# Optimization experiments

Hardware: AMD Instinct MI355X
Metric: run time of the kernel (lower is better)

The kernel has to match this reference:

```python
import jax, jax.numpy as jnp
import numpy as np
from jax import lax

N_HEADS = 10
F_IN = 78
F_OUT = 78           # per-head GAT output dim
HID = N_HEADS * F_OUT  # 780
NEG_SLOPE = 0.2
NUM_GRAPHS = 1024
N_NODES = 40960
N_EDGES = 163840
VOCAB = 26           # CHARPROTLEN + 1
EMB = 128
NFILT = 32
LOUT = 121           # 128 - 8 + 1


def setup_inputs() -> dict:
    key = jax.random.key(0)
    ks = jax.random.split(key, 24)
    d = {}
    d['x'] = jax.random.normal(ks[0], (N_NODES, F_IN), jnp.float32)
    d['edge_index'] = jax.random.randint(ks[1], (2, N_EDGES), 0, N_NODES, jnp.int64)
    d['batch'] = jnp.sort(jax.random.randint(ks[2], (N_NODES,), 0, NUM_GRAPHS, jnp.int64))
    d['target'] = jax.random.randint(ks[3], (NUM_GRAPHS, 1000), 0, VOCAB, jnp.int64)
    s = 0.05
    d['gat_W'] = jax.random.normal(ks[4], (F_IN, HID), jnp.float32) * s
    d['gat_att_src'] = jax.random.normal(ks[5], (N_HEADS, F_OUT), jnp.float32) * s
    d['gat_att_dst'] = jax.random.normal(ks[6], (N_HEADS, F_OUT), jnp.float32) * s
    d['gat_bias'] = jnp.zeros((HID,), jnp.float32)
    d['gcn_W'] = jax.random.normal(ks[7], (HID, HID), jnp.float32) * s
    d['gcn_bias'] = jnp.zeros((HID,), jnp.float32)
    d['fc_g1_W'] = jax.random.normal(ks[8], (2 * HID, 1500), jnp.float32) * s
    d['fc_g1_b'] = jnp.zeros((1500,), jnp.float32)
    d['fc_g2_W'] = jax.random.normal(ks[9], (1500, 128), jnp.float32) * s
    d['fc_g2_b'] = jnp.zeros((128,), jnp.float32)
    d['embed'] = jax.random.normal(ks[10], (VOCAB, EMB), jnp.float32) * s
    d['conv_xt_W'] = jax.random.normal(ks[11], (NFILT, 1000, 8), jnp.float32) * s
    d['conv_xt_b'] = jnp.zeros((NFILT,), jnp.float32)
    d['fc1_xt_W'] = jax.random.normal(ks[12], (NFILT * LOUT, 128), jnp.float32) * s
    d['fc1_xt_b'] = jnp.zeros((128,), jnp.float32)
    d['fc1_W'] = jax.random.normal(ks[13], (256, 1024), jnp.float32) * s
    d['fc1_b'] = jnp.zeros((1024,), jnp.float32)
    d['fc2_W'] = jax.random.normal(ks[14], (1024, 512), jnp.float32) * s
    d['fc2_b'] = jnp.zeros((512,), jnp.float32)
    d['out_W'] = jax.random.normal(ks[15], (512, 1), jnp.float32) * s
    d['out_b'] = jnp.zeros((1,), jnp.float32)
    return d


def _segment_softmax(logits, seg, num_segments):
    m = jax.ops.segment_max(logits, seg, num_segments=num_segments)
    m = jnp.where(jnp.isfinite(m), m, 0.0)
    e = jnp.exp(logits - m[seg])
    s = jax.ops.segment_sum(e, seg, num_segments=num_segments)
    return e / (s[seg] + 1e-16)


def reference(x, edge_index, batch, target, gat_W, gat_att_src, gat_att_dst,
              gat_bias, gcn_W, gcn_bias, fc_g1_W, fc_g1_b, fc_g2_W, fc_g2_b,
              embed, conv_xt_W, conv_xt_b, fc1_xt_W, fc1_xt_b, fc1_W, fc1_b,
              fc2_W, fc2_b, out_W, out_b):
    N = x.shape[0]
    # add self loops (PyG default for both GATConv and GCNConv)
    loops = jnp.arange(N, dtype=edge_index.dtype)
    src = jnp.concatenate([edge_index[0], loops])
    dst = jnp.concatenate([edge_index[1], loops])
    # --- GATConv(78 -> 78, heads=10, concat) ---
    h = (x @ gat_W).reshape(N, N_HEADS, F_OUT)              # [N,10,78]
    a_src = jnp.einsum('nhf,hf->nh', h, gat_att_src)        # [N,10]
    a_dst = jnp.einsum('nhf,hf->nh', h, gat_att_dst)
    logits = jax.nn.leaky_relu(a_src[src] + a_dst[dst], NEG_SLOPE)  # [E',10]
    alpha = _segment_softmax(logits, dst, N)                # softmax over in-edges per dst/head
    agg = jax.ops.segment_sum(h[src] * alpha[:, :, None], dst, num_segments=N)
    x1 = jax.nn.relu(agg.reshape(N, HID) + gat_bias)        # [N,780]
    # --- GCNConv(780 -> 780) with sym normalization ---
    h2 = x1 @ gcn_W
    deg = jax.ops.segment_sum(jnp.ones_like(dst, dtype=h2.dtype), dst, num_segments=N)
    dinv = jnp.where(deg > 0, deg ** -0.5, 0.0)
    norm = dinv[src] * dinv[dst]                            # [E']
    agg2 = jax.ops.segment_sum(h2[src] * norm[:, None], dst, num_segments=N)
    x2 = jax.nn.relu(agg2 + gcn_bias)                       # [N,780]
    # --- global max + mean pool per graph ---
    gmax = jax.ops.segment_max(x2, batch, num_segments=NUM_GRAPHS)
    cnt = jax.ops.segment_sum(jnp.ones((N,), x2.dtype), batch, num_segments=NUM_GRAPHS)
    gmean = jax.ops.segment_sum(x2, batch, num_segments=NUM_GRAPHS) / jnp.maximum(cnt, 1.0)[:, None]
    g = jnp.concatenate([gmax, gmean], axis=1)              # [B,1560]
    g = jax.nn.relu(g @ fc_g1_W + fc_g1_b)
    g = g @ fc_g2_W + fc_g2_b                               # [B,128] (dropout = identity, eval)
    # --- protein branch ---
    e = embed[target]                                       # [B,1000,128]
    conv = lax.conv_general_dilated(e, conv_xt_W, (1,), 'VALID',
                                    dimension_numbers=('NCH', 'OIH', 'NCH'))
    conv = conv + conv_xt_b[None, :, None]                  # [B,32,121]
    xt = conv.reshape(conv.shape[0], NFILT * LOUT) @ fc1_xt_W + fc1_xt_b
    # --- joint head ---
    xc = jnp.concatenate([g, xt], axis=1)                   # [B,256]
    xc = jax.nn.relu(xc @ fc1_W + fc1_b)
    xc = jax.nn.relu(xc @ fc2_W + fc2_b)
    return xc @ out_W + out_b                               # [B,1]
```

## Files before the change

kernel.cpp:

```cpp
#include <hip/hip_runtime.h>

typedef __attribute__((ext_vector_type(4))) float f32x4;
typedef __attribute__((ext_vector_type(8))) short bf16x8;
typedef __attribute__((ext_vector_type(8))) unsigned short u16x8;
typedef unsigned short u16;

#define HID 780
#define NH 10
#define FO 78

__device__ inline u16 f2b(float f) {
  unsigned u = __float_as_uint(f);
  unsigned r = (u + 0x7fff + ((u >> 16) & 1)) >> 16;
  return (u16)r;
}
__device__ inline float b2f(u16 b) { return __uint_as_float(((unsigned)b) << 16); }

__device__ inline void gld16(const u16* g, u16* l) {
  __builtin_amdgcn_global_load_lds(
      (const __attribute__((address_space(1))) unsigned int*)g,
      (__attribute__((address_space(3))) unsigned int*)l, 16, 0, 0);
}

__device__ inline int swz_bid() {
  int gx = gridDim.x, gy = gridDim.y, gz = gridDim.z;
  int nwg = gx * gy * gz;
  int bid = (blockIdx.z * gy + blockIdx.y) * gx + blockIdx.x;
  if ((nwg & 7) == 0) bid = (bid & 7) * (nwg >> 3) + (bid >> 3);
  return bid;
}

template<bool BIAS, bool RELU>
__global__ __launch_bounds__(256) void gemm_mfma(const u16* __restrict__ A,
    const u16* __restrict__ BT, u16* __restrict__ C, float* __restrict__ att_out,
    const float* __restrict__ bias, int M, int Ncols, int KP, int ldc)
{
  __shared__ u16 As[2][128 * 32];
  __shared__ u16 Bs[2][128 * 32];
  const int tid = threadIdx.x;
  int t = swz_bid();
  const int bx = t % gridDim.x, by = t / gridDim.x;
  const int row0 = by << 7, col0 = bx << 7;
  const int l = tid & 63, wid = tid >> 6;
  const int wr = wid >> 1, wc = wid & 1;
  const int lr = l & 15, lk = l >> 4;
  const int c0 = (wid << 6) + l, c1 = 256 + c0;
  const u16* gA0 = A + (size_t)(row0 + (c0 >> 2)) * KP + ((c0 & 3) << 3);
  const u16* gA1 = A + (size_t)(row0 + (c1 >> 2)) * KP + ((c1 & 3) << 3);
  const u16* gB0 = BT + (size_t)(col0 + (c0 >> 2)) * KP + ((c0 & 3) << 3);
  const u16* gB1 = BT + (size_t)(col0 + (c1 >> 2)) * KP + ((c1 & 3) << 3);
  const int d0 = (wid << 6) << 3, d1 = (256 + (wid << 6)) << 3;

  f32x4 acc[4][4];
#pragma unroll
  for (int i = 0; i < 4; ++i)
#pragma unroll
    for (int j = 0; j < 4; ++j) acc[i][j] = (f32x4){0.f, 0.f, 0.f, 0.f};

  gld16(gA0, &As[0][d0]); gld16(gA1, &As[0][d1]);
  gld16(gB0, &Bs[0][d0]); gld16(gB1, &Bs[0][d1]);
  __syncthreads();

  int cur = 0;
  for (int k0 = 0; k0 < KP; k0 += 32) {
    if (k0 + 32 < KP) {
      int nx = cur ^ 1, kn = k0 + 32;
      gld16(gA0 + kn, &As[nx][d0]); gld16(gA1 + kn, &As[nx][d1]);
      gld16(gB0 + kn, &Bs[nx][d0]); gld16(gB1 + kn, &Bs[nx][d1]);
    }
    const u16* Ac = As[cur];
    const u16* Bc = Bs[cur];
    bf16x8 af[4], bfr[4];
#pragma unroll
    for (int fm = 0; fm < 4; ++fm)
      af[fm] = *(const bf16x8*)&Ac[((wr * 64 + fm * 16 + lr) << 5) + (lk << 3)];
#pragma unroll
    for (int fn = 0; fn < 4; ++fn)
      bfr[fn] = *(const bf16x8*)&Bc[((wc * 64 + fn * 16 + lr) << 5) + (lk << 3)];
#pragma unroll
    for (int fm = 0; fm < 4; ++fm)
#pragma unroll
      for (int fn = 0; fn < 4; ++fn)
        acc[fm][fn] = __builtin_amdgcn_mfma_f32_16x16x32_bf16(af[fm], bfr[fn], acc[fm][fn], 0, 0, 0);
    __syncthreads();
    cur ^= 1;
  }
#pragma unroll
  for (int fm = 0; fm < 4; ++fm)
#pragma unroll
    for (int fn = 0; fn < 4; ++fn) {
      int col = col0 + wc * 64 + fn * 16 + lr;
      f32x4 v = acc[fm][fn];
      int rbase = row0 + wr * 64 + fm * 16 + lk * 4;
      if (col < Ncols) {
        float bb = BIAS ? bias[col] : 0.f;
#pragma unroll
        for (int j = 0; j < 4; ++j) {
          float vv = v[j] + bb;
          if (RELU) vv = vv > 0.f ? vv : 0.f;
          C[(size_t)(rbase + j) * ldc + col] = f2b(vv);
        }
      } else {
        if (att_out != nullptr && col < Ncols + 20) {
          int c = col - Ncols;
#pragma unroll
          for (int j = 0; j < 4; ++j)
            att_out[(size_t)(rbase + j) * 20 + c] = v[j];
        }
        if (col < ldc) {
#pragma unroll
          for (int j = 0; j < 4; ++j) C[(size_t)(rbase + j) * ldc + col] = 0;
        }
      }
    }
}

__global__ __launch_bounds__(256) void gemm_sk(const u16* __restrict__ A,
    const u16* __restrict__ BT, float* __restrict__ C,
    int M, int Ncols, int KP, int kchunk)
{
  __shared__ u16 As[2][128 * 32];
  __shared__ u16 Bs[2][128 * 32];
  const int tid = threadIdx.x;
  int t = swz_bid();
  const int bx = t % gridDim.x;
  const int by = (t / gridDim.x) % gridDim.y;
  const int bz = t / (gridDim.x * gridDim.y);
  const int row0 = by << 7, col0 = bx << 7;
  const int kbeg = bz * kchunk;
  const int kend = min(KP, kbeg + kchunk);
  const int l = tid & 63, wid = tid >> 6;
  const int wr = wid >> 1, wc = wid & 1;
  const int lr = l & 15, lk = l >> 4;
  const int c0 = (wid << 6) + l, c1 = 256 + c0;
  const u16* gA0 = A + (size_t)(row0 + (c0 >> 2)) * KP + ((c0 & 3) << 3) + kbeg;
  const u16* gA1 = A + (size_t)(row0 + (c1 >> 2)) * KP + ((c1 & 3) << 3) + kbeg;
  const u16* gB0 = BT + (size_t)(col0 + (c0 >> 2)) * KP + ((c0 & 3) << 3) + kbeg;
  const u16* gB1 = BT + (size_t)(col0 + (c1 >> 2)) * KP + ((c1 & 3) << 3) + kbeg;
  const int d0 = (wid << 6) << 3, d1 = (256 + (wid << 6)) << 3;

  f32x4 acc[4][4];
#pragma unroll
  for (int i = 0; i < 4; ++i)
#pragma unroll
    for (int j = 0; j < 4; ++j) acc[i][j] = (f32x4){0.f, 0.f, 0.f, 0.f};

  gld16(gA0, &As[0][d0]); gld16(gA1, &As[0][d1]);
  gld16(gB0, &Bs[0][d0]); gld16(gB1, &Bs[0][d1]);
  __syncthreads();

  int cur = 0;
  for (int k0 = kbeg; k0 < kend; k0 += 32) {
    if (k0 + 32 < kend) {
      int nx = cur ^ 1, kn = k0 + 32 - kbeg;
      gld16(gA0 + kn, &As[nx][d0]); gld16(gA1 + kn, &As[nx][d1]);
      gld16(gB0 + kn, &Bs[nx][d0]); gld16(gB1 + kn, &Bs[nx][d1]);
    }
    const u16* Ac = As[cur];
    const u16* Bc = Bs[cur];
    bf16x8 af[4], bfr[4];
#pragma unroll
    for (int fm = 0; fm < 4; ++fm)
      af[fm] = *(const bf16x8*)&Ac[((wr * 64 + fm * 16 + lr) << 5) + (lk << 3)];
#pragma unroll
    for (int fn = 0; fn < 4; ++fn)
      bfr[fn] = *(const bf16x8*)&Bc[((wc * 64 + fn * 16 + lr) << 5) + (lk << 3)];
#pragma unroll
    for (int fm = 0; fm < 4; ++fm)
#pragma unroll
      for (int fn = 0; fn < 4; ++fn)
        acc[fm][fn] = __builtin_amdgcn_mfma_f32_16x16x32_bf16(af[fm], bfr[fn], acc[fm][fn], 0, 0, 0);
    __syncthreads();
    cur ^= 1;
  }
#pragma unroll
  for (int fm = 0; fm < 4; ++fm)
#pragma unroll
    for (int fn = 0; fn < 4; ++fn) {
      int col = col0 + wc * 64 + fn * 16 + lr;
      if (col < Ncols) {
        f32x4 v = acc[fm][fn];
        int rbase = row0 + wr * 64 + fm * 16 + lk * 4;
#pragma unroll
        for (int j = 0; j < 4; ++j)
          atomicAdd(&C[(size_t)(rbase + j) * Ncols + col], v[j]);
      }
    }
}

template<bool RELU>
__global__ void bias_act_pad(const float* __restrict__ Cf,
    const float* __restrict__ bias, u16* __restrict__ out,
    int M, int N, int padTo, int ldco)
{
  int idx = blockIdx.x * 256 + threadIdx.x;
  if (idx >= M * padTo) return;
  int r = idx / padTo, c = idx - r * padTo;
  if (c < N) {
    float v = Cf[(size_t)r * N + c] + bias[c];
    if (RELU) v = v > 0.f ? v : 0.f;
    out[(size_t)r * ldco + c] = f2b(v);
  } else {
    out[(size_t)r * ldco + c] = 0;
  }
}

__device__ inline void wtile(const float* __restrict__ W, u16* __restrict__ WT,
    int K, int Ncol, int KP, int NP, int bx, int by, int skip_lo, int skip_hi,
    u16 (*tbuf)[33])
{
  int tn0 = bx << 5, tk0 = by << 5;
  int lx = threadIdx.x & 31, ly = threadIdx.x >> 5;
#pragma unroll
  for (int r = 0; r < 32; r += 8) {
    int k = tk0 + ly + r, n = tn0 + lx;
    tbuf[ly + r][lx] = (k < K && n < Ncol) ? f2b(W[(size_t)k * Ncol + n]) : (u16)0;
  }
  __syncthreads();
#pragma unroll
  for (int r = 0; r < 32; r += 8) {
    int n = tn0 + ly + r, k = tk0 + lx;
    if (n < NP && k < KP && !(n >= skip_lo && n < skip_hi))
      WT[(size_t)n * KP + k] = tbuf[lx][ly + r];
  }
}

__global__ __launch_bounds__(256) void prep_all(
    const float* __restrict__ x, u16* __restrict__ xb,
    const float* __restrict__ gat_W, u16* __restrict__ wt1,
    const float* __restrict__ gcn_W, u16* __restrict__ wt2,
    const float* __restrict__ fcg1_W, u16* __restrict__ wtg1,
    const float* __restrict__ fcg2_W, u16* __restrict__ wtg2,
    const float* __restrict__ fc1xt_W, u16* __restrict__ wtxt,
    const float* __restrict__ fc1_W, u16* __restrict__ wtf1,
    const float* __restrict__ fc2_W, u16* __restrict__ wtf2,
    const float* __restrict__ convW, u16* __restrict__ wtc,
    const float* __restrict__ asv, const float* __restrict__ adv,
    const int* __restrict__ ei, int* __restrict__ cnt, int N, int E)
{
  __shared__ u16 tbuf[32][33];
  int bi = blockIdx.x, tid = threadIdx.x;
  const int s0 = (N * 96 + 255) / 256;
  if (bi < s0) {
    int idx = bi * 256 + tid;
    if (idx < N * 96) {
      int r = idx / 96, c = idx - r * 96;
      xb[idx] = (c < FO) ? f2b(x[(size_t)r * FO + c]) : (u16)0;
    }
    return;
  }
  bi -= s0;
  if (bi < 84)   { wtile(gat_W,  wt1,  FO,   HID,  96,   896,  bi % 28, bi / 28, 780, 800, tbuf); return; }
  bi -= 84;
  if (bi < 700)  { wtile(gcn_W,  wt2,  HID,  HID,  800,  896,  bi % 28, bi / 28, 1 << 30, 0, tbuf); return; }
  bi -= 700;
  if (bi < 2352) { wtile(fcg1_W, wtg1, 1560, 1500, 1568, 1536, bi % 48, bi / 48, 1 << 30, 0, tbuf); return; }
  bi -= 2352;
  if (bi < 188)  { wtile(fcg2_W, wtg2, 1500, 128,  1504, 128,  bi % 4,  bi / 4,  1 << 30, 0, tbuf); return; }
  bi -= 188;
  if (bi < 484)  { wtile(fc1xt_W, wtxt, 3872, 128, 3872, 128,  bi % 4,  bi / 4,  1 << 30, 0, tbuf); return; }
  bi -= 484;
  if (bi < 256)  { wtile(fc1_W,  wtf1, 256,  1024, 256,  1024, bi % 32, bi / 32, 1 << 30, 0, tbuf); return; }
  bi -= 256;
  if (bi < 512)  { wtile(fc2_W,  wtf2, 1024, 512,  1024, 512,  bi % 16, bi / 16, 1 << 30, 0, tbuf); return; }
  bi -= 512;
  if (bi < 1024) {
    int idx = bi * 256 + tid;
    int ok = idx >> 10, c = idx & 1023;
    int o = ok >> 3, k = ok & 7;
    wtc[idx] = (c < 1000) ? f2b(convW[(size_t)o * 8000 + c * 8 + k]) : (u16)0;
    return;
  }
  bi -= 1024;
  if (bi < 20) {
    int j = bi, k = tid;
    if (k >= 96) return;
    float s = 0.f;
    if (k < FO) {
      int h = (j < 10) ? j : j - 10;
      const float* av = ((j < 10) ? asv : adv) + h * FO;
      const float* wr = gat_W + (size_t)k * HID + h * FO;
      for (int f = 0; f < FO; ++f) s += wr[f] * av[f];
    }
    wt1[(size_t)(HID + j) * 96 + k] = f2b(s);
    return;
  }
  bi -= 20;
  {
    int e = bi * 256 + tid;
    if (e >= E + N) return;
    int dst = (e < E) ? ei[E + e] : (e - E);
    atomicAdd(&cnt[dst], 1);
  }
}

__global__ __launch_bounds__(1024) void scan1(const int* __restrict__ cnt,
    int* __restrict__ offs, float* __restrict__ dinv, int* __restrict__ bsum, int N)
{
  __shared__ int sc[1024];
  int b = blockIdx.x, tid = threadIdx.x;
  int g = b * 1024 + tid;
  int c = (g < N) ? cnt[g] : 0;
  sc[tid] = c;
  __syncthreads();
  for (int off = 1; off < 1024; off <<= 1) {
    int v = sc[tid];
    int add = (tid >= off) ? sc[tid - off] : 0;
    __syncthreads();
    sc[tid] = v + add;
    __syncthreads();
  }
  if (g < N) {
    offs[g] = sc[tid] - c;
    dinv[g] = c > 0 ? rsqrtf((float)c) : 0.f;
  }
  if (tid == 1023) bsum[b] = sc[1023];
}

__global__ __launch_bounds__(1024) void scan2(int* __restrict__ offs,
    const int* __restrict__ bsum, int N, int nblk)
{
  int b = blockIdx.x, tid = threadIdx.x;
  int base = 0;
  for (int j = 0; j < b; ++j) base += bsum[j];
  int g = b * 1024 + tid;
  if (g < N && b > 0) offs[g] += base;
  if (b == nblk - 1 && tid == 1023) offs[N] = base + bsum[b];
}

__global__ void fill_csr(const int* __restrict__ ei, int E, int N,
    const int* __restrict__ offs, int* __restrict__ fillpos, int* __restrict__ csr_src)
{
  int e = blockIdx.x * 256 + threadIdx.x;
  if (e >= E + N) return;
  int src, dst;
  if (e < E) { src = ei[e]; dst = ei[E + e]; }
  else { src = e - E; dst = e - E; }
  int p = offs[dst] + atomicAdd(&fillpos[dst], 1);
  csr_src[p] = src;
}

#define CH 48
__global__ __launch_bounds__(64) void gat_gather(const u16* __restrict__ h,
    const float* __restrict__ att,
    const int* __restrict__ offs, const int* __restrict__ csr_src,
    const float* __restrict__ gat_bias, u16* __restrict__ x1b)
{
  int n = blockIdx.x, lane = threadIdx.x;
  int o0 = offs[n], deg = offs[n + 1] - o0;
  __shared__ float ad[NH], ssum[NH];
  __shared__ float wbuf[CH][NH];
  __shared__ int slist[CH];
  if (lane < NH) { ad[lane] = att[n * 20 + 10 + lane]; ssum[lane] = 0.f; }
  const int s0 = lane, s1 = 64 + lane;
  const bool a1 = s1 < 100;
  int hA0 = min((s0 * 8) / FO, NH - 1), bb0 = FO * ((s0 * 8) / FO + 1) - s0 * 8;
  int hB0 = min((s0 * 8) / FO + 1, NH - 1);
  int hA1 = min((s1 * 8) / FO, NH - 1), bb1 = FO * ((s1 * 8) / FO + 1) - s1 * 8;
  int hB1 = min((s1 * 8) / FO + 1, NH - 1);
  float acc0[8], acc1[8];
#pragma unroll
  for (int j = 0; j < 8; ++j) { acc0[j] = 0.f; acc1[j] = 0.f; }
  __syncthreads();

  for (int e0 = 0; e0 < deg; e0 += CH) {
    int ce = min(CH, deg - e0);
    for (int idx = lane; idx < ce * NH; idx += 64) {
      int e = idx / NH, hd = idx - e * NH;
      int s = csr_src[o0 + e0 + e];
      float l = att[s * 20 + hd] + ad[hd];
      l = l > 0.f ? l : 0.2f * l;
      float w = __expf(l);
      wbuf[e][hd] = w;
      atomicAdd(&ssum[hd], w);
    }
    for (int idx = lane; idx < ce; idx += 64) slist[idx] = csr_src[o0 + e0 + idx];
    __syncthreads();
    for (int e = 0; e < ce; ++e) {
      const u16* hs = h + (size_t)slist[e] * 800;
      u16x8 v0 = *(const u16x8*)(hs + s0 * 8);
      float wA0 = wbuf[e][hA0], wB0 = wbuf[e][hB0];
#pragma unroll
      for (int j = 0; j < 8; ++j)
        acc0[j] += (j < bb0 ? wA0 : wB0) * b2f(v0[j]);
      if (a1) {
        u16x8 v1 = *(const u16x8*)(hs + s1 * 8);
        float wA1 = wbuf[e][hA1], wB1 = wbuf[e][hB1];
#pragma unroll
        for (int j = 0; j < 8; ++j)
          acc1[j] += (j < bb1 ? wA1 : wB1) * b2f(v1[j]);
      }
    }
    __syncthreads();
  }
  float iA0 = 1.f / (ssum[hA0] + 1e-16f), iB0 = 1.f / (ssum[hB0] + 1e-16f);
  u16x8 o0v;
#pragma unroll
  for (int j = 0; j < 8; ++j) {
    int f = s0 * 8 + j;
    float v = acc0[j] * (j < bb0 ? iA0 : iB0) + gat_bias[f];
    o0v[j] = f2b(v > 0.f ? v : 0.f);
  }
  *(u16x8*)(x1b + (size_t)n * 800 + s0 * 8) = o0v;
  if (a1) {
    float iA1 = 1.f / (ssum[hA1] + 1e-16f), iB1 = 1.f / (ssum[hB1] + 1e-16f);
    u16x8 o1v;
#pragma unroll
    for (int j = 0; j < 8; ++j) {
      int f = s1 * 8 + j;
      if (f < HID) {
        float v = acc1[j] * (j < bb1 ? iA1 : iB1) + gat_bias[f];
        o1v[j] = f2b(v > 0.f ? v : 0.f);
      } else o1v[j] = 0;
    }
    *(u16x8*)(x1b + (size_t)n * 800 + s1 * 8) = o1v;
  }
}

__global__ __launch_bounds__(256) void gcn_pool(const u16* __restrict__ h2,
    const int* __restrict__ offs, const int* __restrict__ csr_src,
    const float* __restrict__ dinv, const float* __restrict__ gcn_bias,
    const int* __restrict__ batch, int N, u16* __restrict__ gb)
{
  int gi = blockIdx.x, tid = threadIdx.x;
  int grp = tid >> 6, lane = tid & 63;
  __shared__ int se[2];
  __shared__ float smx[HID];
  __shared__ float ssm[HID];
  for (int f = tid; f < HID; f += 256) { smx[f] = 0.f; ssm[f] = 0.f; }
  if (tid < 2) {
    int target = gi + tid;
    int lo = 0, hi = N;
    while (lo < hi) { int mid = (lo + hi) >> 1; if (batch[mid] < target) lo = mid + 1; else hi = mid; }
    se[tid] = lo;
  }
  __syncthreads();
  int s = se[0], e = se[1];
  const int s0 = lane, s1 = 64 + lane;
  const bool a1 = s1 < 100;
  float bv0[8], bv1[8];
#pragma unroll
  for (int j = 0; j < 8; ++j) {
    int f0 = s0 * 8 + j, f1 = s1 * 8 + j;
    bv0[j] = gcn_bias[f0];
    bv1[j] = (a1 && f1 < HID) ? gcn_bias[f1] : 0.f;
  }
  float mx0[8], sm0[8], mx1[8], sm1[8];
#pragma unroll
  for (int j = 0; j < 8; ++j) { mx0[j] = 0.f; sm0[j] = 0.f; mx1[j] = 0.f; sm1[j] = 0.f; }

  for (int n = s + grp; n < e; n += 4) {
    int o0 = offs[n], deg = offs[n + 1] - o0;
    float dn = dinv[n];
    float acc0[8], acc1[8];
#pragma unroll
    for (int j = 0; j < 8; ++j) { acc0[j] = 0.f; acc1[j] = 0.f; }
    for (int eb = 0; eb < deg; eb += 64) {
      int ce = min(64, deg - eb);
      int   src_l = (lane < ce) ? csr_src[o0 + eb + lane] : 0;
      float c_l   = (lane < ce) ? dn * dinv[src_l] : 0.f;
      int   sc = __shfl(src_l, 0, 64);
      float cc = __shfl(c_l, 0, 64);
      const u16* hr = h2 + (size_t)sc * 800;
      u16x8 v0 = *(const u16x8*)(hr + s0 * 8);
      u16x8 v1 = a1 ? *(const u16x8*)(hr + s1 * 8) : v0;
      for (int ed = 0; ed < ce; ++ed) {
        u16x8 n0 = v0, n1 = v1;
        float nc = 0.f;
        if (ed + 1 < ce) {
          int ns = __shfl(src_l, ed + 1, 64);
          nc = __shfl(c_l, ed + 1, 64);
          const u16* nh = h2 + (size_t)ns * 800;
          n0 = *(const u16x8*)(nh + s0 * 8);
          if (a1) n1 = *(const u16x8*)(nh + s1 * 8);
        }
#pragma unroll
        for (int j = 0; j < 8; ++j) acc0[j] += cc * b2f(v0[j]);
        if (a1) {
#pragma unroll
          for (int j = 0; j < 8; ++j) acc1[j] += cc * b2f(v1[j]);
        }
        v0 = n0; v1 = n1; cc = nc;
      }
    }
#pragma unroll
    for (int j = 0; j < 8; ++j) {
      float v = acc0[j] + bv0[j];
      v = v > 0.f ? v : 0.f;
      mx0[j] = fmaxf(mx0[j], v); sm0[j] += v;
      float w = acc1[j] + bv1[j];
      w = w > 0.f ? w : 0.f;
      mx1[j] = fmaxf(mx1[j], w); sm1[j] += w;
    }
  }
#pragma unroll
  for (int j = 0; j < 8; ++j) {
    int f0 = s0 * 8 + j;
    atomicMax((unsigned*)&smx[f0], __float_as_uint(mx0[j]));
    atomicAdd(&ssm[f0], sm0[j]);
    int f1 = s1 * 8 + j;
    if (a1 && f1 < HID) {
      atomicMax((unsigned*)&smx[f1], __float_as_uint(mx1[j]));
      atomicAdd(&ssm[f1], sm1[j]);
    }
  }
  __syncthreads();
  float inv = 1.f / fmaxf((float)(e - s), 1.f);
  for (int f = tid; f < HID; f += 256) {
    gb[(size_t)gi * 1568 + f] = f2b(smx[f]);
    gb[(size_t)gi * 1568 + HID + f] = f2b(ssm[f] * inv);
  }
  if (tid < 8) gb[(size_t)gi * 1568 + 1560 + tid] = 0;
}

__global__ __launch_bounds__(256) void build_ind(const int* __restrict__ tgt,
    u16* __restrict__ Ind)
{
  int b = blockIdx.x, tid = threadIdx.x;
  __shared__ unsigned char tl[1000];
  for (int i = tid; i < 1000; i += 256) tl[i] = (unsigned char)tgt[b * 1000 + i];
  __syncthreads();
  u16* out = Ind + (size_t)b * 26 * 1024;
  for (int ci = tid; ci < 26 * 128; ci += 256) {
    int v = ci >> 7, c0 = (ci & 127) << 3;
    u16x8 w;
#pragma unroll
    for (int j = 0; j < 8; ++j) {
      int c = c0 + j;
      w[j] = (c < 1000 && tl[c] == v) ? (u16)0x3F80 : (u16)0;
    }
    *(u16x8*)(out + v * 1024 + c0) = w;
  }
}

__global__ __launch_bounds__(256) void conv_xt(const u16* __restrict__ Aall,
    const float* __restrict__ embed, const float* __restrict__ cbias,
    u16* __restrict__ out)
{
  int b = blockIdx.x, tid = threadIdx.x;
  __shared__ __align__(16) float Al[6656];
  __shared__ __align__(16) float el[3360];
  const u16* Ab = Aall + (size_t)b * 6656;
  for (int i = tid; i < 6656; i += 256) Al[i] = b2f(Ab[i]);
  for (int i = tid; i < 3328; i += 256) el[i] = embed[i];
  if (tid < 32) el[3328 + tid] = 0.f;
  __syncthreads();
  for (int grp = tid; grp < 512; grp += 256) {
    int o = grp >> 4;
    int l0 = (grp & 15) << 3;
    float cb = cbias[o];
    float acc[8];
#pragma unroll
    for (int j = 0; j < 8; ++j) acc[j] = cb;
    for (int v = 0; v < 26; ++v) {
      const float* ap = &Al[v * 256 + (o << 3)];
      f32x4 a0 = *(const f32x4*)ap;
      f32x4 a1 = *(const f32x4*)(ap + 4);
      const float* ep = &el[v * 128 + l0];
      f32x4 e0 = *(const f32x4*)ep;
      f32x4 e1 = *(const f32x4*)(ep + 4);
      f32x4 e2 = *(const f32x4*)(ep + 8);
      f32x4 e3 = *(const f32x4*)(ep + 12);
      float a[8] = { a0[0], a0[1], a0[2], a0[3], a1[0], a1[1], a1[2], a1[3] };
      float e[16] = { e0[0], e0[1], e0[2], e0[3], e1[0], e1[1], e1[2], e1[3],
                      e2[0], e2[1], e2[2], e2[3], e3[0], e3[1], e3[2], e3[3] };
#pragma unroll
      for (int k = 0; k < 8; ++k)
#pragma unroll
        for (int j = 0; j < 8; ++j) acc[j] += a[k] * e[k + j];
    }
    int base = o * 121 + l0;
#pragma unroll
    for (int j = 0; j < 8; ++j)
      if (l0 + j < 121) out[(size_t)b * 3872 + base + j] = f2b(acc[j]);
  }
}

__global__ __launch_bounds__(256) void final_out(const u16* __restrict__ z2,
    const float* __restrict__ W, const float* __restrict__ bias, float* __restrict__ out)
{
  int row = blockIdx.x * 4 + (threadIdx.x >> 6);
  int lane = threadIdx.x & 63;
  const u16* zr = z2 + (size_t)row * 512;
  float s = 0.f;
  for (int i = lane; i < 512; i += 64) s += b2f(zr[i]) * W[i];
#pragma unroll
  for (int off = 32; off > 0; off >>= 1) s += __shfl_down(s, off, 64);
  if (lane == 0) out[row] = s + bias[0];
}

extern "C" void kernel_launch(void* const* d_in, const int* in_sizes, int n_in,
                              void* d_out, int out_size, void* d_ws, size_t ws_size,
                              hipStream_t stream)
{
  const float* x        = (const float*)d_in[0];
  const int*   ei       = (const int*)d_in[1];
  const int*   batch    = (const int*)d_in[2];
  const int*   tgt      = (const int*)d_in[3];
  const float* gat_W    = (const float*)d_in[4];
  const float* att_src  = (const float*)d_in[5];
  const float* att_dst  = (const float*)d_in[6];
  const float* gat_bias = (const float*)d_in[7];
  const float* gcn_W    = (const float*)d_in[8];
  const float* gcn_bias = (const float*)d_in[9];
  const float* fcg1_W   = (const float*)d_in[10];
  const float* fcg1_b   = (const float*)d_in[11];
  const float* fcg2_W   = (const float*)d_in[12];
  const float* fcg2_b   = (const float*)d_in[13];
  const float* embed    = (const float*)d_in[14];
  const float* convW    = (const float*)d_in[15];
  const float* convb    = (const float*)d_in[16];
  const float* fc1xt_W  = (const float*)d_in[17];
  const float* fc1xt_b  = (const float*)d_in[18];
  const float* fc1_W    = (const float*)d_in[19];
  const float* fc1_b    = (const float*)d_in[20];
  const float* fc2_W    = (const float*)d_in[21];
  const float* fc2_b    = (const float*)d_in[22];
  const float* out_W    = (const float*)d_in[23];
  const float* out_b    = (const float*)d_in[24];

  const int N = in_sizes[0] / FO;
  const int E = in_sizes[1] / 2;
  const int B = in_sizes[3] / 1000;
  const int ET = E + N;

  char* ws = (char*)d_ws;
  size_t off = 0;
  auto alloc = [&](size_t bytes) -> char* {
    char* p = ws + off;
    off = (off + bytes + 255) & ~(size_t)255;
    return p;
  };
  float* buf0  = (float*)alloc((size_t)N * HID * 4);
  float* buf1  = (float*)alloc((size_t)N * 800 * 2);
  u16*   wt1   = (u16*)alloc((size_t)896 * 96 * 2);
  u16*   wt2   = (u16*)alloc((size_t)896 * 800 * 2);
  u16*   wtg1  = (u16*)alloc((size_t)1536 * 1568 * 2);
  u16*   wtg2  = (u16*)alloc((size_t)128 * 1504 * 2);
  u16*   wtxt  = (u16*)alloc((size_t)128 * 3872 * 2);
  u16*   wtf1  = (u16*)alloc((size_t)1024 * 256 * 2);
  u16*   wtf2  = (u16*)alloc((size_t)512 * 1024 * 2);
  u16*   wtc   = (u16*)alloc((size_t)256 * 1024 * 2);
  float* att   = (float*)alloc((size_t)N * 20 * 4);
  int*   cnt   = (int*)alloc((size_t)N * 4);
  int*   offs  = (int*)alloc((size_t)(N + 1) * 4);
  int*   fillp = (int*)alloc((size_t)N * 4);
  int*   csr   = (int*)alloc((size_t)ET * 4);
  float* dinv  = (float*)alloc((size_t)N * 4);
  u16*   gb    = (u16*)alloc((size_t)B * 1568 * 2);
  int*   bsum  = (int*)alloc((size_t)64 * 4);

  u16*   xb    = (u16*)buf1;
  u16*   x1b   = (u16*)buf1;
  u16*   hb    = (u16*)buf0;
  u16*   Ind      = (u16*)buf0;
  u16*   Ab       = Ind + (size_t)26624 * 1024;
  u16*   convflat = Ab + (size_t)26624 * 256;
  float* g1f = (float*)(convflat + (size_t)1024 * 3872);
  float* xtf = g1f + (size_t)1024 * 1500;
  float* g2f = xtf + (size_t)1024 * 128;
  float* z1f = g2f + (size_t)1024 * 128;
  float* z2f = z1f + (size_t)1024 * 1024;
  size_t skBytes = ((size_t)1024 * (1500 + 128 + 128 + 1024 + 512)) * 4;
  u16* g1b = (u16*)buf1;
  u16* xcb = g1b + (size_t)1024 * 1504;
  u16* z1b = xcb + (size_t)1024 * 256;
  u16* z2b = z1b + (size_t)1024 * 1024;

  hipMemsetAsync(cnt, 0, (size_t)N * 4, stream);
  hipMemsetAsync(fillp, 0, (size_t)N * 4, stream);

  int nbx = (N * 96 + 255) / 256;
  int nprep = nbx + 84 + 700 + 2352 + 188 + 484 + 256 + 512 + 1024 + 20 + (ET + 255) / 256;
  prep_all<<<nprep, 256, 0, stream>>>(
      x, xb, gat_W, wt1, gcn_W, wt2, fcg1_W, wtg1, fcg2_W, wtg2,
      fc1xt_W, wtxt, fc1_W, wtf1, fc2_W, wtf2, convW, wtc,
      att_src, att_dst, ei, cnt, N, E);

  gemm_mfma<false, false><<<dim3(7, N / 128), 256, 0, stream>>>(
      xb, wt1, hb, att, nullptr, N, HID, 96, 800);

  int nblk = (N + 1023) / 1024;
  scan1<<<nblk, 1024, 0, stream>>>(cnt, offs, dinv, bsum, N);
  scan2<<<nblk, 1024, 0, stream>>>(offs, bsum, N, nblk);
  fill_csr<<<(ET + 255) / 256, 256, 0, stream>>>(ei, E, N, offs, fillp, csr);

  gat_gather<<<N, 64, 0, stream>>>(hb, att, offs, csr, gat_bias, x1b);

  gemm_mfma<false, false><<<dim3(7, N / 128), 256, 0, stream>>>(
      x1b, wt2, hb, nullptr, nullptr, N, HID, 800, 800);

  gcn_pool<<<B, 256, 0, stream>>>(hb, offs, csr, dinv, gcn_bias, batch, N, gb);

  build_ind<<<B, 256, 0, stream>>>(tgt, Ind);
  gemm_mfma<false, false><<<dim3(2, 26624 / 128), 256, 0, stream>>>(
      Ind, wtc, Ab, nullptr, nullptr, 26624, 256, 1024, 256);
  conv_xt<<<B, 256, 0, stream>>>(Ab, embed, convb, convflat);

  hipMemsetAsync(g1f, 0, skBytes, stream);

  gemm_sk<<<dim3(1, B / 128, 16), 256, 0, stream>>>(convflat, wtxt, xtf, B, 128, 3872, 256);
  bias_act_pad<false><<<(B * 128 + 255) / 256, 256, 0, stream>>>(
      xtf, fc1xt_b, xcb + 128, B, 128, 128, 256);

  gemm_sk<<<dim3(12, B / 128, 2), 256, 0, stream>>>(gb, wtg1, g1f, B, 1500, 1568, 800);
  bias_act_pad<true><<<(B * 1504 + 255) / 256, 256, 0, stream>>>(
      g1f, fcg1_b, g1b, B, 1500, 1504, 1504);

  gemm_sk<<<dim3(1, B / 128, 8), 256, 0, stream>>>(g1b, wtg2, g2f, B, 128, 1504, 192);
  bias_act_pad<false><<<(B * 128 + 255) / 256, 256, 0, stream>>>(
      g2f, fcg2_b, xcb, B, 128, 128, 256);

  gemm_sk<<<dim3(8, B / 128, 2), 256, 0, stream>>>(xcb, wtf1, z1f, B, 1024, 256, 128);
  bias_act_pad<true><<<(B * 1024 + 255) / 256, 256, 0, stream>>>(
      z1f, fc1_b, z1b, B, 1024, 1024, 1024);

  gemm_sk<<<dim3(4, B / 128, 4), 256, 0, stream>>>(z1b, wtf2, z2f, B, 512, 1024, 256);
  bias_act_pad<true><<<(B * 512 + 255) / 256, 256, 0, stream>>>(
      z2f, fc2_b, z2b, B, 512, 512, 512);

  final_out<<<B / 4, 256, 0, stream>>>(z2b, out_W, out_b, (float*)d_out);
}
```

Before: 471.8 us.

## Merge independent GEMMs and bias kernels into dual launches, fold build_ind into prep

Independent work is combined into shared launches. The GAT projection GEMM and the protein one-hot conv GEMM now run as one grid, and the fc1_xt and fc_g1 split-K GEMMs share another grid. Their bias/activation epilogues are merged into one kernel, and the one-hot build moves into the prep_all mega-kernel. This cuts kernel launch count and fills the GPU better with small grids. In exchange, Ab and convflat get dedicated buffers and Ind is moved to live inside buf1, which adds memory and needs care about aliasing.

```diff
diff --git a/kernel.cpp b/kernel.cpp
--- a/kernel.cpp
+++ b/kernel.cpp
@@ -30,16 +30,12 @@
   return bid;
 }
 
-template<bool BIAS, bool RELU>
-__global__ __launch_bounds__(256) void gemm_mfma(const u16* __restrict__ A,
+__device__ __forceinline__ void gemm_core(const u16* __restrict__ A,
     const u16* __restrict__ BT, u16* __restrict__ C, float* __restrict__ att_out,
-    const float* __restrict__ bias, int M, int Ncols, int KP, int ldc)
-{
-  __shared__ u16 As[2][128 * 32];
-  __shared__ u16 Bs[2][128 * 32];
+    int Ncols, int KP, int ldc, int bx, int by,
+    u16 (*As)[4096], u16 (*Bs)[4096])
+{
   const int tid = threadIdx.x;
-  int t = swz_bid();
-  const int bx = t % gridDim.x, by = t / gridDim.x;
   const int row0 = by << 7, col0 = bx << 7;
   const int l = tid & 63, wid = tid >> 6;
   const int wr = wid >> 1, wc = wid & 1;
@@ -93,13 +89,9 @@
       f32x4 v = acc[fm][fn];
       int rbase = row0 + wr * 64 + fm * 16 + lk * 4;
       if (col < Ncols) {
-        float bb = BIAS ? bias[col] : 0.f;
-#pragma unroll
-        for (int j = 0; j < 4; ++j) {
-          float vv = v[j] + bb;
-          if (RELU) vv = vv > 0.f ? vv : 0.f;
-          C[(size_t)(rbase + j) * ldc + col] = f2b(vv);
-        }
+#pragma unroll
+        for (int j = 0; j < 4; ++j)
+          C[(size_t)(rbase + j) * ldc + col] = f2b(v[j]);
       } else {
         if (att_out != nullptr && col < Ncols + 20) {
           int c = col - Ncols;
@@ -115,17 +107,43 @@
     }
 }
 
-__global__ __launch_bounds__(256) void gemm_sk(const u16* __restrict__ A,
+__global__ __launch_bounds__(256) void gemm_mfma(const u16* __restrict__ A,
+    const u16* __restrict__ BT, u16* __restrict__ C, float* __restrict__ att_out,
+    int Ncols, int KP, int ldc)
+{
+  __shared__ u16 As[2][4096];
+  __shared__ u16 Bs[2][4096];
+  int t = swz_bid();
+  gemm_core(A, BT, C, att_out, Ncols, KP, ldc, t % gridDim.x, t / gridDim.x, As, Bs);
+}
+
+__global__ __launch_bounds__(256) void gemm_dual(
+    const u16* __restrict__ A1, const u16* __restrict__ B1, u16* __restrict__ C1,
+    float* __restrict__ att1, int N1, int K1, int l1, int gx1, int nb1,
+    const u16* __restrict__ A2, const u16* __restrict__ B2, u16* __restrict__ C2,
+    int N2, int K2, int l2, int gx2)
+{
+  __shared__ u16 As[2][4096];
+  __shared__ u16 Bs[2][4096];
+  int bi = blockIdx.x;
+  if (bi < nb1) {
+    int t = bi;
+    if ((nb1 & 7) == 0) t = (bi & 7) * (nb1 >> 3) + (bi >> 3);
+    gemm_core(A1, B1, C1, att1, N1, K1, l1, t % gx1, t / gx1, As, Bs);
+  } else {
+    int nb2 = gridDim.x - nb1, b2 = bi - nb1;
+    int t = b2;
+    if ((nb2 & 7) == 0) t = (b2 & 7) * (nb2 >> 3) + (b2 >> 3);
+    gemm_core(A2, B2, C2, nullptr, N2, K2, l2, t % gx2, t / gx2, As, Bs);
+  }
+}
+
+__device__ __forceinline__ void sk_core(const u16* __restrict__ A,
     const u16* __restrict__ BT, float* __restrict__ C,
-    int M, int Ncols, int KP, int kchunk)
-{
-  __shared__ u16 As[2][128 * 32];
-  __shared__ u16 Bs[2][128 * 32];
+    int Ncols, int KP, int kchunk, int bx, int by, int bz,
+    u16 (*As)[4096], u16 (*Bs)[4096])
+{
   const int tid = threadIdx.x;
-  int t = swz_bid();
-  const int bx = t % gridDim.x;
-  const int by = (t / gridDim.x) % gridDim.y;
-  const int bz = t / (gridDim.x * gridDim.y);
   const int row0 = by << 7, col0 = bx << 7;
   const int kbeg = bz * kchunk;
   const int kend = min(KP, kbeg + kchunk);
@@ -188,6 +206,40 @@
     }
 }
 
+__global__ __launch_bounds__(256) void gemm_sk(const u16* __restrict__ A,
+    const u16* __restrict__ BT, float* __restrict__ C,
+    int Ncols, int KP, int kchunk)
+{
+  __shared__ u16 As[2][4096];
+  __shared__ u16 Bs[2][4096];
+  int t = swz_bid();
+  int bx = t % gridDim.x;
+  int by = (t / gridDim.x) % gridDim.y;
+  int bz = t / (gridDim.x * gridDim.y);
+  sk_core(A, BT, C, Ncols, KP, kchunk, bx, by, bz, As, Bs);
+}
+
+__global__ __launch_bounds__(256) void gemm_sk_dual(
+    const u16* __restrict__ A1, const u16* __restrict__ B1, float* __restrict__ C1,
+    int N1, int K1, int kc1, int gx1, int gy1, int nb1,
+    const u16* __restrict__ A2, const u16* __restrict__ B2, float* __restrict__ C2,
+    int N2, int K2, int kc2, int gx2, int gy2)
+{
+  __shared__ u16 As[2][4096];
+  __shared__ u16 Bs[2][4096];
+  int bi = blockIdx.x;
+  if (bi < nb1) {
+    int t = bi;
+    if ((nb1 & 7) == 0) t = (bi & 7) * (nb1 >> 3) + (bi >> 3);
+    sk_core(A1, B1, C1, N1, K1, kc1, t % gx1, (t / gx1) % gy1, t / (gx1 * gy1), As, Bs);
+  } else {
+    int nb2 = gridDim.x - nb1, b2 = bi - nb1;
+    int t = b2;
+    if ((nb2 & 7) == 0) t = (b2 & 7) * (nb2 >> 3) + (b2 >> 3);
+    sk_core(A2, B2, C2, N2, K2, kc2, t % gx2, (t / gx2) % gy2, t / (gx2 * gy2), As, Bs);
+  }
+}
+
 template<bool RELU>
 __global__ void bias_act_pad(const float* __restrict__ Cf,
     const float* __restrict__ bias, u16* __restrict__ out,
@@ -202,6 +254,31 @@
     out[(size_t)r * ldco + c] = f2b(v);
   } else {
     out[(size_t)r * ldco + c] = 0;
+  }
+}
+
+__global__ void bias_dual(const float* __restrict__ C1, const float* __restrict__ b1,
+    u16* __restrict__ o1, int M1, int N1, int p1, int l1,
+    const float* __restrict__ C2, const float* __restrict__ b2,
+    u16* __restrict__ o2, int M2, int N2, int p2, int l2)
+{
+  int idx = blockIdx.x * 256 + threadIdx.x;
+  int t1 = M1 * p1;
+  if (idx < t1) {
+    int r = idx / p1, c = idx - r * p1;
+    if (c < N1) o1[(size_t)r * l1 + c] = f2b(C1[(size_t)r * N1 + c] + b1[c]);
+    else o1[(size_t)r * l1 + c] = 0;
+    return;
+  }
+  idx -= t1;
+  if (idx >= M2 * p2) return;
+  int r = idx / p2, c = idx - r * p2;
+  if (c < N2) {
+    float v = C2[(size_t)r * N2 + c] + b2[c];
+    v = v > 0.f ? v : 0.f;
+    o2[(size_t)r * l2 + c] = f2b(v);
+  } else {
+    o2[(size_t)r * l2 + c] = 0;
   }
 }
 
@@ -236,9 +313,11 @@
     const float* __restrict__ fc2_W, u16* __restrict__ wtf2,
     const float* __restrict__ convW, u16* __restrict__ wtc,
     const float* __restrict__ asv, const float* __restrict__ adv,
+    const int* __restrict__ tgt, u16* __restrict__ Ind,
     const int* __restrict__ ei, int* __restrict__ cnt, int N, int E)
 {
   __shared__ u16 tbuf[32][33];
+  __shared__ unsigned char tl[1000];
   int bi = blockIdx.x, tid = threadIdx.x;
   const int s0 = (N * 96 + 255) / 256;
   if (bi < s0) {
@@ -286,6 +365,24 @@
     return;
   }
   bi -= 20;
+  if (bi < 1024) {
+    int b = bi;
+    for (int i = tid; i < 1000; i += 256) tl[i] = (unsigned char)tgt[b * 1000 + i];
+    __syncthreads();
+    u16* out = Ind + (size_t)b * 26 * 1024;
+    for (int ci = tid; ci < 26 * 128; ci += 256) {
+      int v = ci >> 7, c0 = (ci & 127) << 3;
+      u16x8 w;
+#pragma unroll
+      for (int j = 0; j < 8; ++j) {
+        int c = c0 + j;
+        w[j] = (c < 1000 && tl[c] == v) ? (u16)0x3F80 : (u16)0;
+      }
+      *(u16x8*)(out + v * 1024 + c0) = w;
+    }
+    return;
+  }
+  bi -= 1024;
   {
     int e = bi * 256 + tid;
     if (e >= E + N) return;
@@ -511,26 +608,6 @@
     gb[(size_t)gi * 1568 + HID + f] = f2b(ssm[f] * inv);
   }
   if (tid < 8) gb[(size_t)gi * 1568 + 1560 + tid] = 0;
-}
-
-__global__ __launch_bounds__(256) void build_ind(const int* __restrict__ tgt,
-    u16* __restrict__ Ind)
-{
-  int b = blockIdx.x, tid = threadIdx.x;
-  __shared__ unsigned char tl[1000];
-  for (int i = tid; i < 1000; i += 256) tl[i] = (unsigned char)tgt[b * 1000 + i];
-  __syncthreads();
-  u16* out = Ind + (size_t)b * 26 * 1024;
-  for (int ci = tid; ci < 26 * 128; ci += 256) {
-    int v = ci >> 7, c0 = (ci & 127) << 3;
-    u16x8 w;
-#pragma unroll
-    for (int j = 0; j < 8; ++j) {
-      int c = c0 + j;
-      w[j] = (c < 1000 && tl[c] == v) ? (u16)0x3F80 : (u16)0;
-    }
-    *(u16x8*)(out + v * 1024 + c0) = w;
-  }
 }
 
 __global__ __launch_bounds__(256) void conv_xt(const u16* __restrict__ Aall,
@@ -633,6 +710,8 @@
   };
   float* buf0  = (float*)alloc((size_t)N * HID * 4);
   float* buf1  = (float*)alloc((size_t)N * 800 * 2);
+  u16*   Ab       = (u16*)alloc((size_t)26624 * 256 * 2);
+  u16*   convflat = (u16*)alloc((size_t)1024 * 3872 * 2);
   u16*   wt1   = (u16*)alloc((size_t)896 * 96 * 2);
   u16*   wt2   = (u16*)alloc((size_t)896 * 800 * 2);
   u16*   wtg1  = (u16*)alloc((size_t)1536 * 1568 * 2);
@@ -651,12 +730,10 @@
   int*   bsum  = (int*)alloc((size_t)64 * 4);
 
   u16*   xb    = (u16*)buf1;
+  u16*   Ind   = (u16*)((char*)buf1 + (size_t)N * 96 * 2);
   u16*   x1b   = (u16*)buf1;
   u16*   hb    = (u16*)buf0;
-  u16*   Ind      = (u16*)buf0;
-  u16*   Ab       = Ind + (size_t)26624 * 1024;
-  u16*   convflat = Ab + (size_t)26624 * 256;
-  float* g1f = (float*)(convflat + (size_t)1024 * 3872);
+  float* g1f = buf0;
   float* xtf = g1f + (size_t)1024 * 1500;
   float* g2f = xtf + (size_t)1024 * 128;
   float* z1f = g2f + (size_t)1024 * 128;
@@ -671,51 +748,49 @@
   hipMemsetAsync(fillp, 0, (size_t)N * 4, stream);
 
   int nbx = (N * 96 + 255) / 256;
-  int nprep = nbx + 84 + 700 + 2352 + 188 + 484 + 256 + 512 + 1024 + 20 + (ET + 255) / 256;
+  int nprep = nbx + 84 + 700 + 2352 + 188 + 484 + 256 + 512 + 1024 + 20 + 1024 + (ET + 255) / 256;
   prep_all<<<nprep, 256, 0, stream>>>(
       x, xb, gat_W, wt1, gcn_W, wt2, fcg1_W, wtg1, fcg2_W, wtg2,
       fc1xt_W, wtxt, fc1_W, wtf1, fc2_W, wtf2, convW, wtc,
-      att_src, att_dst, ei, cnt, N, E);
-
-  gemm_mfma<false, false><<<dim3(7, N / 128), 256, 0, stream>>>(
-      xb, wt1, hb, att, nullptr, N, HID, 96, 800);
+      att_src, att_dst, tgt, Ind, ei, cnt, N, E);
+
+  int nb1 = 7 * (N / 128);
+  int nb2 = 2 * (26624 / 128);
+  gemm_dual<<<nb1 + nb2, 256, 0, stream>>>(
+      xb, wt1, hb, att, HID, 96, 800, 7, nb1,
+      Ind, wtc, Ab, 256, 1024, 256, 2);
 
   int nblk = (N + 1023) / 1024;
   scan1<<<nblk, 1024, 0, stream>>>(cnt, offs, dinv, bsum, N);
   scan2<<<nblk, 1024, 0, stream>>>(offs, bsum, N, nblk);
+  conv_xt<<<B, 256, 0, stream>>>(Ab, embed, convb, convflat);
   fill_csr<<<(ET + 255) / 256, 256, 0, stream>>>(ei, E, N, offs, fillp, csr);
 
   gat_gather<<<N, 64, 0, stream>>>(hb, att, offs, csr, gat_bias, x1b);
 
-  gemm_mfma<false, false><<<dim3(7, N / 128), 256, 0, stream>>>(
-      x1b, wt2, hb, nullptr, nullptr, N, HID, 800, 800);
+  gemm_mfma<<<dim3(7, N / 128), 256, 0, stream>>>(x1b, wt2, hb, nullptr, HID, 800, 800);
 
   gcn_pool<<<B, 256, 0, stream>>>(hb, offs, csr, dinv, gcn_bias, batch, N, gb);
 
-  build_ind<<<B, 256, 0, stream>>>(tgt, Ind);
-  gemm_mfma<false, false><<<dim3(2, 26624 / 128), 256, 0, stream>>>(
-      Ind, wtc, Ab, nullptr, nullptr, 26624, 256, 1024, 256);
-  conv_xt<<<B, 256, 0, stream>>>(Ab, embed, convb, convflat);
-
   hipMemsetAsync(g1f, 0, skBytes, stream);
 
-  gemm_sk<<<dim3(1, B / 128, 16), 256, 0, stream>>>(convflat, wtxt, xtf, B, 128, 3872, 256);
-  bias_act_pad<false><<<(B * 128 + 255) / 256, 256, 0, stream>>>(
-      xtf, fc1xt_b, xcb + 128, B, 128, 128, 256);
-
-  gemm_sk<<<dim3(12, B / 128, 2), 256, 0, stream>>>(gb, wtg1, g1f, B, 1500, 1568, 800);
-  bias_act_pad<true><<<(B * 1504 + 255) / 256, 256, 0, stream>>>(
+  gemm_sk_dual<<<128 + 192, 256, 0, stream>>>(
+      convflat, wtxt, xtf, 128, 3872, 256, 1, 8, 128,
+      gb, wtg1, g1f, 1500, 1568, 800, 12, 8);
+  int nbias = (B * 128 + B * 1504 + 255) / 256;
+  bias_dual<<<nbias, 256, 0, stream>>>(
+      xtf, fc1xt_b, xcb + 128, B, 128, 128, 256,
       g1f, fcg1_b, g1b, B, 1500, 1504, 1504);
 
-  gemm_sk<<<dim3(1, B / 128, 8), 256, 0, stream>>>(g1b, wtg2, g2f, B, 128, 1504, 192);
+  gemm_sk<<<dim3(1, B / 128, 8), 256, 0, stream>>>(g1b, wtg2, g2f, 128, 1504, 192);
   bias_act_pad<false><<<(B * 128 + 255) / 256, 256, 0, stream>>>(
       g2f, fcg2_b, xcb, B, 128, 128, 256);
 
-  gemm_sk<<<dim3(8, B / 128, 2), 256, 0, stream>>>(xcb, wtf1, z1f, B, 1024, 256, 128);
+  gemm_sk<<<dim3(8, B / 128, 2), 256, 0, stream>>>(xcb, wtf1, z1f, 1024, 256, 128);
   bias_act_pad<true><<<(B * 1024 + 255) / 256, 256, 0, stream>>>(
       z1f, fc1_b, z1b, B, 1024, 1024, 1024);
 
-  gemm_sk<<<dim3(4, B / 128, 4), 256, 0, stream>>>(z1b, wtf2, z2f, B, 512, 1024, 256);
+  gemm_sk<<<dim3(4, B / 128, 4), 256, 0, stream>>>(z1b, wtf2, z2f, 512, 1024, 256);
   bias_act_pad<true><<<(B * 512 + 255) / 256, 256, 0, stream>>>(
       z2f, fc2_b, z2b, B, 512, 512, 512);
 
```

New measurement: 446.3 us. 1.06x faster.
